# Performance work log

Hardware: AMD Instinct MI355X
Metric: run time of the kernel (lower is better)

The kernel has to match this reference:

```python
import jax, jax.numpy as jnp
import numpy as np

B, C_IN, C_OUT, H, W = 4, 128, 64, 64, 64


def setup_inputs() -> dict:
    key = jax.random.key(0)
    ks = jax.random.split(key, 10)
    s = 0.05
    return {
        "x": jax.random.normal(ks[0], (B, C_IN, H, W), dtype=jnp.float32),
        "Wf": jax.random.normal(ks[1], (C_OUT, C_IN), dtype=jnp.float32) * s,
        "bf": jax.random.normal(ks[2], (C_OUT,), dtype=jnp.float32) * s,
        "Wg": jax.random.normal(ks[3], (C_OUT, C_IN), dtype=jnp.float32) * s,
        "bg": jax.random.normal(ks[4], (C_OUT,), dtype=jnp.float32) * s,
        "Wh": jax.random.normal(ks[5], (C_OUT, C_IN), dtype=jnp.float32) * s,
        "bh": jax.random.normal(ks[6], (C_OUT,), dtype=jnp.float32) * s,
        "Wa": jax.random.normal(ks[7], (C_OUT, C_OUT), dtype=jnp.float32) * s,
        "ba": jax.random.normal(ks[8], (C_OUT,), dtype=jnp.float32) * s,
        "gamma": jnp.ones((1,), dtype=jnp.float32),
    }


def _conv1x1(W, b, xf):
    # xf: [B, Cin, N] -> [B, Cout, N]
    return jnp.einsum('oc,bcn->bon', W, xf) + b[None, :, None]


def reference(x, Wf, bf, Wg, bg, Wh, bh, Wa, ba, gamma):
    nb, nc, imgh, imgw = x.shape
    xf = x.reshape(nb, nc, imgh * imgw)            # [B, Cin, N]
    f = _conv1x1(Wf, bf, xf)                       # [B, Co, N]
    g = _conv1x1(Wg, bg, xf)
    h = _conv1x1(Wh, bh, xf)
    # s = f^T @ g : [B, N, N]
    s = jnp.einsum('bon,bom->bnm', f, g)
    beta = jax.nn.softmax(s, axis=-1)              # softmax over keys (last dim)
    # o = beta @ h^T : [B, N, Co]
    o = jnp.einsum('bnm,bom->bno', beta, h)
    o = jnp.swapaxes(o, 1, 2)                      # [B, Co, N]
    o = _conv1x1(Wa, ba, o)                        # attn_conv 1x1
    out = gamma * o.reshape(nb, -1, imgh, imgw)    # [B, Co, H, W]
    return out
```

## Files before the change

### kernel.cpp

```cpp
#include <hip/hip_runtime.h>
#include <math.h>

#define BATCH 4
#define CIN   128
#define CO    64
#define NPIX  4096
#define LOG2E 1.4426950408889634f

typedef unsigned int   uint_t;
typedef unsigned short ushort_t;
typedef __bf16 bfx8 __attribute__((ext_vector_type(8)));
typedef float  f32x4  __attribute__((ext_vector_type(4)));
typedef float  f32x16 __attribute__((ext_vector_type(16)));

#define MFMA(a,b,c)   __builtin_amdgcn_mfma_f32_16x16x32_bf16((a),(b),(c),0,0,0)
#define MFMA32(a,b,c) __builtin_amdgcn_mfma_f32_32x32x16_bf16((a),(b),(c),0,0,0)
#define BC8(x) __builtin_bit_cast(bfx8,(x))

#if __has_builtin(__builtin_amdgcn_exp2f)
#define EXP2(x) __builtin_amdgcn_exp2f(x)
#else
#define EXP2(x) exp2f(x)
#endif

static __device__ __forceinline__ ushort_t f2bf(float f) {
    uint_t u = __builtin_bit_cast(uint_t, f);
    u = (u + 0x7fffu + ((u >> 16) & 1u)) >> 16;
    return (ushort_t)u;
}
static __device__ __forceinline__ float bf2f(ushort_t h) {
    return __builtin_bit_cast(float, (uint_t)h << 16);
}
static __device__ __forceinline__ uint_t pk2(float a, float b) {
    return (uint_t)f2bf(a) | ((uint_t)f2bf(b) << 16);
}
static __device__ __forceinline__ uint_t cvtpk(float lo, float hi) {
    uint_t r;
    asm("v_cvt_pk_bf16_f32 %0, %1, %2" : "=v"(r) : "v"(lo), "v"(hi));
    return r;
}
static __device__ __forceinline__ void gload16(const void* g, void* l) {
    __builtin_amdgcn_global_load_lds(
        (const __attribute__((address_space(1))) void*)g,
        (__attribute__((address_space(3))) void*)l, 16, 0, 0);
}

__global__ __launch_bounds__(256) void wconv_kernel(
    const float* __restrict__ Wf, const float* __restrict__ Wg,
    const float* __restrict__ Wh, const float* __restrict__ Wa,
    ushort_t* __restrict__ Wb)
{
    int gid = blockIdx.x * 256 + threadIdx.x;
    for (int e = gid; e < 28672; e += 4096) {
        float v;
        if      (e < 8192)  v = Wf[e];
        else if (e < 16384) v = Wg[e - 8192];
        else if (e < 24576) v = Wh[e - 16384];
        else                v = Wa[e - 24576];
        Wb[e] = f2bf(v);
    }
}

__global__ __launch_bounds__(256) void proj_kernel(
    const float* __restrict__ x, const ushort_t* __restrict__ Wb,
    const float* __restrict__ bf_, const float* __restrict__ bg_, const float* __restrict__ bh_,
    ushort_t* __restrict__ Q, ushort_t* __restrict__ K, ushort_t* __restrict__ V)
{
    int bid = blockIdx.x, b = bid >> 6, n0 = (bid & 63) << 6, t = threadIdx.x;
    int w = t >> 6, lane = t & 63, cl = lane & 15, g = (lane >> 4) & 3;

    const float* xcol = x + (size_t)b * CIN * NPIX + n0 + (w << 4) + cl;

    uint4 aq[4], al[4];
    #pragma unroll
    for (int ks = 0; ks < 4; ++ks) {
        float v[8];
        #pragma unroll
        for (int j = 0; j < 8; ++j)
            v[j] = xcol[(size_t)((ks << 5) + (g << 3) + j) * NPIX];
        ushort_t hv[8];
        #pragma unroll
        for (int j = 0; j < 8; ++j) hv[j] = f2bf(v[j]);
        uint4 a, l;
        a.x = (uint_t)hv[0] | ((uint_t)hv[1] << 16);
        a.y = (uint_t)hv[2] | ((uint_t)hv[3] << 16);
        a.z = (uint_t)hv[4] | ((uint_t)hv[5] << 16);
        a.w = (uint_t)hv[6] | ((uint_t)hv[7] << 16);
        l.x = pk2(v[0] - bf2f(hv[0]), v[1] - bf2f(hv[1]));
        l.y = pk2(v[2] - bf2f(hv[2]), v[3] - bf2f(hv[3]));
        l.z = pk2(v[4] - bf2f(hv[4]), v[5] - bf2f(hv[5]));
        l.w = pk2(v[6] - bf2f(hv[6]), v[7] - bf2f(hv[7]));
        aq[ks] = a; al[ks] = l;
    }

    const float* bps[3] = {bf_, bg_, bh_};
    int nb = n0 + (w << 4);

    for (int p = 0; p < 3; ++p) {
        const ushort_t* Wp = Wb + p * 8192;
        float sc = (p == 0) ? LOG2E : 1.0f;
        f32x4 acc[4];
        #pragma unroll
        for (int ot = 0; ot < 4; ++ot) acc[ot] = (f32x4){0.f,0.f,0.f,0.f};
        #pragma unroll
        for (int ks = 0; ks < 4; ++ks) {
            #pragma unroll
            for (int ot = 0; ot < 4; ++ot) {
                uint4 bq = *(const uint4*)(Wp + (((ot << 4) + cl) << 7) + (ks << 5) + (g << 3));
                acc[ot] = MFMA(BC8(aq[ks]), BC8(bq), acc[ot]);
                acc[ot] = MFMA(BC8(al[ks]), BC8(bq), acc[ot]);
            }
        }
        if (p < 2) {
            ushort_t* dst = (p == 0 ? Q : K) + ((size_t)b * NPIX + nb) * CO;
            #pragma unroll
            for (int ot = 0; ot < 4; ++ot) {
                float bias = bps[p][(ot << 4) + cl];
                #pragma unroll
                for (int r = 0; r < 4; ++r)
                    dst[(size_t)((g << 2) + r) * CO + (ot << 4) + cl] = f2bf((acc[ot][r] + bias) * sc);
            }
        } else {
            #pragma unroll
            for (int ot = 0; ot < 4; ++ot) {
                float bias = bps[p][(ot << 4) + cl];
                uint2 pk;
                pk.x = pk2(acc[ot][0] + bias, acc[ot][1] + bias);
                pk.y = pk2(acc[ot][2] + bias, acc[ot][3] + bias);
                ushort_t* Vd = V + (size_t)b * CO * NPIX + (size_t)((ot << 4) + cl) * NPIX + nb + (g << 2);
                *(uint2*)Vd = pk;
            }
        }
    }
}

__global__ __launch_bounds__(1024, 4) void flash_kernel(
    const ushort_t* __restrict__ Q, const ushort_t* __restrict__ K,
    const ushort_t* __restrict__ V, const ushort_t* __restrict__ Wb,
    const float* __restrict__ ba, const float* __restrict__ gamma,
    float* __restrict__ out)
{
    extern __shared__ __align__(16) char smem[];

    int orig = blockIdx.x;
    int bid = ((orig & 7) << 5) | (orig >> 3);
    int b = bid >> 6, n0 = (bid & 63) << 6, t = threadIdx.x;
    int w = t >> 6, lane = t & 63;
    int qh = w >> 3, ks = w & 7;
    int ql = lane & 31, hi = lane >> 5;

    const ushort_t* Qb = Q + ((size_t)b * NPIX + n0) * CO;
    const ushort_t* Kb = K + (size_t)b * NPIX * CO;
    const ushort_t* Vb = V + (size_t)b * CO * NPIX;

    int q = (qh << 5) + ql;
    uint4 qf[4];
    #pragma unroll
    for (int m = 0; m < 4; ++m)
        qf[m] = *(const uint4*)(Qb + q * CO + (m << 4) + (hi << 3));

    f32x16 oac0 = (f32x16)0.f, oac1 = (f32x16)0.f;
    float mreg = -INFINITY, lreg = 0.f;

    int kl = (ql & 19) | ((ql & 4) << 1) | ((ql & 8) >> 1);
    int key = (ks << 5) + kl;
    int koff[4];
    #pragma unroll
    for (int m = 0; m < 4; ++m)
        koff[m] = (key << 7) + (((((m << 1) | hi)) ^ (key & 7)) << 4);
    int voff[2][2];
    #pragma unroll
    for (int dh = 0; dh < 2; ++dh)
        #pragma unroll
        for (int kt = 0; kt < 2; ++kt) {
            int dv = (dh << 5) + ql;
            int slot = (((ks << 2) + (kt << 1) + hi)) ^ (dv & 7);
            voff[dh][kt] = 32768 + (dv << 9) + (slot << 4);
        }

    auto STAGE = [&](char* buf, int kt) {
        #pragma unroll
        for (int i = 0; i < 2; ++i) {
            int cb = (i << 10) + (w << 6);
            int ci = cb | lane;
            int kk = ci >> 3, kc = (ci & 7) ^ (kk & 7);
            gload16(Kb + (size_t)((kt << 8) + kk) * CO + (kc << 3), buf + (cb << 4));
            int d = ci >> 5, vc = (ci & 31) ^ (d & 7);
            gload16(Vb + (size_t)d * NPIX + (kt << 8) + (vc << 3), buf + 32768 + (cb << 4));
        }
    };

    auto DOTILE = [&](char* bufc) {
        uint4 kf0 = *(const uint4*)(bufc + koff[0]);
        uint4 kf1 = *(const uint4*)(bufc + koff[1]);
        uint4 kf2 = *(const uint4*)(bufc + koff[2]);
        uint4 kf3 = *(const uint4*)(bufc + koff[3]);
        f32x16 s = (f32x16)0.f;
        __builtin_amdgcn_s_setprio(1);
        s = MFMA32(BC8(kf0), BC8(qf[0]), s);
        s = MFMA32(BC8(kf1), BC8(qf[1]), s);
        s = MFMA32(BC8(kf2), BC8(qf[2]), s);
        s = MFMA32(BC8(kf3), BC8(qf[3]), s);
        __builtin_amdgcn_s_setprio(0);

        float mx = s[0];
        #pragma unroll
        for (int p = 1; p < 16; ++p) mx = fmaxf(mx, s[p]);
        mx = fmaxf(mx, __shfl_xor(mx, 32));
        if (!__all(mx <= mreg + 11.5f)) {
            float mn = fmaxf(mreg, mx);
            float r  = EXP2(mreg - mn);
            lreg *= r;
            oac0 *= r; oac1 *= r;
            mreg = mn;
        }
        float pv[16], ls = 0.f;
        #pragma unroll
        for (int p = 0; p < 16; ++p) { pv[p] = EXP2(s[p] - mreg); ls += pv[p]; }
        ls += __shfl_xor(ls, 32);
        lreg += ls;
        uint4 pb0, pb1;
        pb0.x = cvtpk(pv[0], pv[1]);  pb0.y = cvtpk(pv[2],  pv[3]);
        pb0.z = cvtpk(pv[4], pv[5]);  pb0.w = cvtpk(pv[6],  pv[7]);
        pb1.x = cvtpk(pv[8], pv[9]);  pb1.y = cvtpk(pv[10], pv[11]);
        pb1.z = cvtpk(pv[12], pv[13]); pb1.w = cvtpk(pv[14], pv[15]);

        uint4 vf00 = *(const uint4*)(bufc + voff[0][0]);
        uint4 vf01 = *(const uint4*)(bufc + voff[0][1]);
        uint4 vf10 = *(const uint4*)(bufc + voff[1][0]);
        uint4 vf11 = *(const uint4*)(bufc + voff[1][1]);
        __builtin_amdgcn_s_setprio(1);
        oac0 = MFMA32(BC8(vf00), BC8(pb0), oac0);
        oac0 = MFMA32(BC8(vf01), BC8(pb1), oac0);
        oac1 = MFMA32(BC8(vf10), BC8(pb0), oac1);
        oac1 = MFMA32(BC8(vf11), BC8(pb1), oac1);
        __builtin_amdgcn_s_setprio(0);
    };

    STAGE(smem, 0);
    __syncthreads();
    for (int i = 0; i < 16; ++i) {
        if (i + 1 < 16) STAGE(smem + (((i + 1) & 1) << 16), i + 1);
        DOTILE(smem + ((i & 1) << 16));
        __syncthreads();
    }

    float* mlb = (float*)(smem + 131072);
    float* llb = (float*)(smem + 133120);
    if (lane < 32) {
        mlb[(w << 5) + lane] = mreg;
        llb[(w << 5) + lane] = lreg;
    }
    __syncthreads();

    float M = -INFINITY;
    float mv[8];
    #pragma unroll
    for (int i = 0; i < 8; ++i) {
        mv[i] = mlb[(((qh << 3) + i) << 5) + ql];
        M = fmaxf(M, mv[i]);
    }
    float L = 0.f;
    #pragma unroll
    for (int i = 0; i < 8; ++i)
        L += EXP2(mv[i] - M) * llb[(((qh << 3) + i) << 5) + ql];
    float fac = EXP2(mreg - M) / L;
    oac0 *= fac; oac1 *= fac;

    for (int r = 0; r < 7; ++r) {
        if (ks == r) {
            #pragma unroll
            for (int dh = 0; dh < 2; ++dh)
                #pragma unroll
                for (int j2 = 0; j2 < 4; ++j2) {
                    int slot = (((j2 << 1) + hi + (dh << 3))) ^ (q & 7);
                    int off = (q << 8) + (slot << 4);
                    f32x4 v;
                    if (dh == 0) v = (f32x4){oac0[4*j2], oac0[4*j2+1], oac0[4*j2+2], oac0[4*j2+3]};
                    else         v = (f32x4){oac1[4*j2], oac1[4*j2+1], oac1[4*j2+2], oac1[4*j2+3]};
                    if (r > 0) v += *(const f32x4*)(smem + off);
                    *(f32x4*)(smem + off) = v;
                }
        }
        __syncthreads();
    }
    ushort_t* Pb = (ushort_t*)(smem + 16384);
    if (ks == 7) {
        #pragma unroll
        for (int dh = 0; dh < 2; ++dh)
            #pragma unroll
            for (int j2 = 0; j2 < 4; ++j2) {
                int slot = (((j2 << 1) + hi + (dh << 3))) ^ (q & 7);
                int off = (q << 8) + (slot << 4);
                f32x4 v;
                if (dh == 0) v = (f32x4){oac0[4*j2], oac0[4*j2+1], oac0[4*j2+2], oac0[4*j2+3]};
                else         v = (f32x4){oac1[4*j2], oac1[4*j2+1], oac1[4*j2+2], oac1[4*j2+3]};
                v += *(const f32x4*)(smem + off);
                uint2 pk;
                pk.x = pk2(v[0], v[1]);
                pk.y = pk2(v[2], v[3]);
                *(uint2*)((char*)Pb + q * 144 + (j2 << 4) + (hi << 3) + (dh << 6)) = pk;
            }
    }
    __syncthreads();

    {
        int c = lane & 15, g = (lane >> 4) & 3;
        const ushort_t* Wab = Wb + 24576;
        float gm = gamma[0];
        int ot = w >> 2, qt3 = w & 3;
        f32x4 acc2 = (f32x4){0.f,0.f,0.f,0.f};
        #pragma unroll
        for (int k2 = 0; k2 < 2; ++k2) {
            uint4 af  = *(const uint4*)(Wab + (((ot << 4) + c) << 6) + (k2 << 5) + (g << 3));
            uint4 pfq = *(const uint4*)((char*)Pb + (((qt3 << 4) + c)) * 144 + (k2 << 6) + (g << 4));
            acc2 = MFMA(BC8(af), BC8(pfq), acc2);
        }
        float* ob = out + (size_t)b * CO * NPIX + n0;
        #pragma unroll
        for (int r = 0; r < 4; ++r) {
            int o = (ot << 4) + (g << 2) + r;
            ob[(size_t)o * NPIX + (qt3 << 4) + c] = gm * (acc2[r] + ba[o]);
        }
    }
}

extern "C" void kernel_launch(void* const* d_in, const int* in_sizes, int n_in,
                              void* d_out, int out_size, void* d_ws, size_t ws_size,
                              hipStream_t stream) {
    const float* x     = (const float*)d_in[0];
    const float* Wf    = (const float*)d_in[1];
    const float* bf_   = (const float*)d_in[2];
    const float* Wg    = (const float*)d_in[3];
    const float* bg_   = (const float*)d_in[4];
    const float* Wh    = (const float*)d_in[5];
    const float* bh_   = (const float*)d_in[6];
    const float* Wa    = (const float*)d_in[7];
    const float* ba    = (const float*)d_in[8];
    const float* gamma = (const float*)d_in[9];
    float* out = (float*)d_out;

    ushort_t* Wb = (ushort_t*)d_ws;
    const size_t matb = (size_t)BATCH * NPIX * CO;
    ushort_t* Q = (ushort_t*)((char*)d_ws + 65536);
    ushort_t* K = Q + matb;
    ushort_t* V = K + matb;

    wconv_kernel<<<16, 256, 0, stream>>>(Wf, Wg, Wh, Wa, Wb);
    proj_kernel<<<BATCH * (NPIX / 64), 256, 0, stream>>>(x, Wb, bf_, bg_, bh_, Q, K, V);
    flash_kernel<<<BATCH * (NPIX / 64), 1024, 135168, stream>>>(Q, K, V, Wb, ba, gamma, out);
}
```

Before: 54.02 us.

## Split flash attention over key halves with merge kernel; drop bf16 residual projection

The flash kernel now splits the key dimension in two, launching twice as many blocks. Each block writes a partial output plus its max and sum, and a new merge kernel combines the two halves and applies the output 1x1 conv. Shared memory per block is halved by dropping double buffering, so more blocks can fit per CU. The projection also stops using the hi/lo bf16 split of x, which halves its MFMAs at the cost of precision. Writing the partials and running an extra launch adds global traffic and the K/V loads are no longer overlapped with compute.

```diff
diff --git a/kernel.cpp b/kernel.cpp
--- a/kernel.cpp
+++ b/kernel.cpp
@@ -71,26 +71,19 @@
 
     const float* xcol = x + (size_t)b * CIN * NPIX + n0 + (w << 4) + cl;
 
-    uint4 aq[4], al[4];
+    uint4 aq[4];
     #pragma unroll
     for (int ks = 0; ks < 4; ++ks) {
         float v[8];
         #pragma unroll
         for (int j = 0; j < 8; ++j)
             v[j] = xcol[(size_t)((ks << 5) + (g << 3) + j) * NPIX];
-        ushort_t hv[8];
-        #pragma unroll
-        for (int j = 0; j < 8; ++j) hv[j] = f2bf(v[j]);
-        uint4 a, l;
-        a.x = (uint_t)hv[0] | ((uint_t)hv[1] << 16);
-        a.y = (uint_t)hv[2] | ((uint_t)hv[3] << 16);
-        a.z = (uint_t)hv[4] | ((uint_t)hv[5] << 16);
-        a.w = (uint_t)hv[6] | ((uint_t)hv[7] << 16);
-        l.x = pk2(v[0] - bf2f(hv[0]), v[1] - bf2f(hv[1]));
-        l.y = pk2(v[2] - bf2f(hv[2]), v[3] - bf2f(hv[3]));
-        l.z = pk2(v[4] - bf2f(hv[4]), v[5] - bf2f(hv[5]));
-        l.w = pk2(v[6] - bf2f(hv[6]), v[7] - bf2f(hv[7]));
-        aq[ks] = a; al[ks] = l;
+        uint4 a;
+        a.x = pk2(v[0], v[1]);
+        a.y = pk2(v[2], v[3]);
+        a.z = pk2(v[4], v[5]);
+        a.w = pk2(v[6], v[7]);
+        aq[ks] = a;
     }
 
     const float* bps[3] = {bf_, bg_, bh_};
@@ -108,7 +101,6 @@
             for (int ot = 0; ot < 4; ++ot) {
                 uint4 bq = *(const uint4*)(Wp + (((ot << 4) + cl) << 7) + (ks << 5) + (g << 3));
                 acc[ot] = MFMA(BC8(aq[ks]), BC8(bq), acc[ot]);
-                acc[ot] = MFMA(BC8(al[ks]), BC8(bq), acc[ot]);
             }
         }
         if (p < 2) {
@@ -136,15 +128,16 @@
 
 __global__ __launch_bounds__(1024, 4) void flash_kernel(
     const ushort_t* __restrict__ Q, const ushort_t* __restrict__ K,
-    const ushort_t* __restrict__ V, const ushort_t* __restrict__ Wb,
-    const float* __restrict__ ba, const float* __restrict__ gamma,
-    float* __restrict__ out)
+    const ushort_t* __restrict__ V,
+    ushort_t* __restrict__ PartO, float* __restrict__ PartS)
 {
     extern __shared__ __align__(16) char smem[];
 
     int orig = blockIdx.x;
-    int bid = ((orig & 7) << 5) | (orig >> 3);
-    int b = bid >> 6, n0 = (bid & 63) << 6, t = threadIdx.x;
+    int bid2 = ((orig & 7) << 6) | (orig >> 3);
+    int half = bid2 >> 8, bq = bid2 & 255;
+    int b = bq >> 6, n0 = (bq & 63) << 6;
+    int t = threadIdx.x;
     int w = t >> 6, lane = t & 63;
     int qh = w >> 3, ks = w & 7;
     int ql = lane & 31, hi = lane >> 5;
@@ -179,14 +172,15 @@
         }
 
     auto STAGE = [&](char* buf, int kt) {
+        int kb = (half << 11) + (kt << 8);
         #pragma unroll
         for (int i = 0; i < 2; ++i) {
             int cb = (i << 10) + (w << 6);
             int ci = cb | lane;
             int kk = ci >> 3, kc = (ci & 7) ^ (kk & 7);
-            gload16(Kb + (size_t)((kt << 8) + kk) * CO + (kc << 3), buf + (cb << 4));
+            gload16(Kb + (size_t)(kb + kk) * CO + (kc << 3), buf + (cb << 4));
             int d = ci >> 5, vc = (ci & 31) ^ (d & 7);
-            gload16(Vb + (size_t)d * NPIX + (kt << 8) + (vc << 3), buf + 32768 + (cb << 4));
+            gload16(Vb + (size_t)d * NPIX + kb + (vc << 3), buf + 32768 + (cb << 4));
         }
     };
 
@@ -237,16 +231,15 @@
         __builtin_amdgcn_s_setprio(0);
     };
 
-    STAGE(smem, 0);
-    __syncthreads();
-    for (int i = 0; i < 16; ++i) {
-        if (i + 1 < 16) STAGE(smem + (((i + 1) & 1) << 16), i + 1);
-        DOTILE(smem + ((i & 1) << 16));
+    for (int i = 0; i < 8; ++i) {
+        STAGE(smem, i);
         __syncthreads();
-    }
-
-    float* mlb = (float*)(smem + 131072);
-    float* llb = (float*)(smem + 133120);
+        DOTILE(smem);
+        __syncthreads();
+    }
+
+    float* mlb = (float*)(smem + 65536);
+    float* llb = (float*)(smem + 67584);
     if (lane < 32) {
         mlb[(w << 5) + lane] = mreg;
         llb[(w << 5) + lane] = lreg;
@@ -264,7 +257,7 @@
     #pragma unroll
     for (int i = 0; i < 8; ++i)
         L += EXP2(mv[i] - M) * llb[(((qh << 3) + i) << 5) + ql];
-    float fac = EXP2(mreg - M) / L;
+    float fac = EXP2(mreg - M);
     oac0 *= fac; oac1 *= fac;
 
     for (int r = 0; r < 7; ++r) {
@@ -284,8 +277,9 @@
         }
         __syncthreads();
     }
-    ushort_t* Pb = (ushort_t*)(smem + 16384);
+    int pidx = (half << 8) | bq;
     if (ks == 7) {
+        ushort_t* PO = PartO + (size_t)pidx * 4096;
         #pragma unroll
         for (int dh = 0; dh < 2; ++dh)
             #pragma unroll
@@ -299,27 +293,72 @@
                 uint2 pk;
                 pk.x = pk2(v[0], v[1]);
                 pk.y = pk2(v[2], v[3]);
-                *(uint2*)((char*)Pb + q * 144 + (j2 << 4) + (hi << 3) + (dh << 6)) = pk;
+                int d0 = (j2 << 3) + (hi << 2) + (dh << 5);
+                *(uint2*)(PO + q * 64 + d0) = pk;
             }
-    }
+        if (hi == 0) {
+            PartS[pidx * 128 + q]      = M;
+            PartS[pidx * 128 + 64 + q] = L;
+        }
+    }
+}
+
+__global__ __launch_bounds__(256) void merge_kernel(
+    const ushort_t* __restrict__ PartO, const float* __restrict__ PartS,
+    const ushort_t* __restrict__ Wb, const float* __restrict__ ba,
+    const float* __restrict__ gamma, float* __restrict__ out)
+{
+    __shared__ ushort_t Pb[64][72];
+
+    int bid = blockIdx.x;
+    int b = bid >> 6, n0 = (bid & 63) << 6;
+    int t = threadIdx.x;
+    int pidx0 = bid, pidx1 = 256 + bid;
+
+    int q = t >> 2, dc = (t & 3) << 4;
+    float M0 = PartS[pidx0 * 128 + q], L0 = PartS[pidx0 * 128 + 64 + q];
+    float M1 = PartS[pidx1 * 128 + q], L1 = PartS[pidx1 * 128 + 64 + q];
+    float M  = fmaxf(M0, M1);
+    float a0 = EXP2(M0 - M), a1 = EXP2(M1 - M);
+    float inv = 1.0f / (a0 * L0 + a1 * L1);
+    a0 *= inv; a1 *= inv;
+
+    const ushort_t* p0 = PartO + (size_t)pidx0 * 4096 + q * 64 + dc;
+    const ushort_t* p1 = PartO + (size_t)pidx1 * 4096 + q * 64 + dc;
+    uint4 u0a = *(const uint4*)p0, u0b = *(const uint4*)(p0 + 8);
+    uint4 u1a = *(const uint4*)p1, u1b = *(const uint4*)(p1 + 8);
+
+    auto comb = [&](uint_t x0, uint_t x1) -> uint_t {
+        float lo = a0 * bf2f((ushort_t)(x0 & 0xffffu)) + a1 * bf2f((ushort_t)(x1 & 0xffffu));
+        float hh = a0 * bf2f((ushort_t)(x0 >> 16))     + a1 * bf2f((ushort_t)(x1 >> 16));
+        return pk2(lo, hh);
+    };
+    uint4 w0, w1;
+    w0.x = comb(u0a.x, u1a.x); w0.y = comb(u0a.y, u1a.y);
+    w0.z = comb(u0a.z, u1a.z); w0.w = comb(u0a.w, u1a.w);
+    w1.x = comb(u0b.x, u1b.x); w1.y = comb(u0b.y, u1b.y);
+    w1.z = comb(u0b.z, u1b.z); w1.w = comb(u0b.w, u1b.w);
+    ushort_t* dst = &Pb[q][dc];
+    *(uint4*)dst       = w0;
+    *(uint4*)(dst + 8) = w1;
     __syncthreads();
 
-    {
-        int c = lane & 15, g = (lane >> 4) & 3;
-        const ushort_t* Wab = Wb + 24576;
-        float gm = gamma[0];
-        int ot = w >> 2, qt3 = w & 3;
+    int w_ = t >> 6, lane = t & 63, c = lane & 15, g = (lane >> 4) & 3;
+    const ushort_t* Wab = Wb + 24576;
+    float gm = gamma[0];
+    float* ob = out + (size_t)b * CO * NPIX + n0;
+    #pragma unroll
+    for (int qt3 = 0; qt3 < 4; ++qt3) {
         f32x4 acc2 = (f32x4){0.f,0.f,0.f,0.f};
         #pragma unroll
         for (int k2 = 0; k2 < 2; ++k2) {
-            uint4 af  = *(const uint4*)(Wab + (((ot << 4) + c) << 6) + (k2 << 5) + (g << 3));
+            uint4 af  = *(const uint4*)(Wab + (((w_ << 4) + c) << 6) + (k2 << 5) + (g << 3));
             uint4 pfq = *(const uint4*)((char*)Pb + (((qt3 << 4) + c)) * 144 + (k2 << 6) + (g << 4));
             acc2 = MFMA(BC8(af), BC8(pfq), acc2);
         }
-        float* ob = out + (size_t)b * CO * NPIX + n0;
         #pragma unroll
         for (int r = 0; r < 4; ++r) {
-            int o = (ot << 4) + (g << 2) + r;
+            int o = (w_ << 4) + (g << 2) + r;
             ob[(size_t)o * NPIX + (qt3 << 4) + c] = gm * (acc2[r] + ba[o]);
         }
     }
@@ -345,8 +384,11 @@
     ushort_t* Q = (ushort_t*)((char*)d_ws + 65536);
     ushort_t* K = Q + matb;
     ushort_t* V = K + matb;
+    ushort_t* PartO = (ushort_t*)((char*)d_ws + 65536 + 6291456);
+    float*    PartS = (float*)((char*)d_ws + 65536 + 6291456 + 4194304);
 
     wconv_kernel<<<16, 256, 0, stream>>>(Wf, Wg, Wh, Wa, Wb);
     proj_kernel<<<BATCH * (NPIX / 64), 256, 0, stream>>>(x, Wb, bf_, bg_, bh_, Q, K, V);
-    flash_kernel<<<BATCH * (NPIX / 64), 1024, 135168, stream>>>(Q, K, V, Wb, ba, gamma, out);
-}
+    flash_kernel<<<2 * BATCH * (NPIX / 64), 1024, 69632, stream>>>(Q, K, V, PartO, PartS);
+    merge_kernel<<<BATCH * (NPIX / 64), 256, 0, stream>>>(PartO, PartS, Wb, ba, gamma, out);
+}
```

Measured after the change: 64.25 us. 18.9% more time.
